# Optimization experiments

Hardware: AMD Instinct MI355X
Metric: run time of the kernel (lower is better)

## Reference

```python
import jax, jax.numpy as jnp
import numpy as np

G = 0.001
EPS = 1e-6


def setup_inputs() -> dict:
    key = jax.random.key(0)
    k1, k2 = jax.random.split(key)
    B, N, D = 8, 4096, 3
    q = jax.random.normal(k1, (B, N, D), dtype=jnp.float32)
    m = jax.random.uniform(k2, (N,), dtype=jnp.float32)
    return {"q": q, "m": m}


def reference(q, m):
    # q: (B, N, D), m: (N,)
    N = q.shape[-2]
    diff = q[:, :, None, :] - q[:, None, :, :]          # (B, N, N, D)
    dist = jnp.sqrt(jnp.sum(diff * diff, axis=-1) + EPS)  # (B, N, N)
    mass_matrix = m[:, None] * m[None, :]                # (N, N)
    V = -G * mass_matrix / dist                          # (B, N, N)
    # zero the diagonal (self-interaction), matching fill_(0.0)
    off_diag = 1.0 - jnp.eye(N, dtype=q.dtype)
    V = V * off_diag
    return jnp.sum(V, axis=(-1, -2)) / 2.0               # (B,)
```

## Files before the change

### kernel.cpp

```cpp
#include <hip/hip_runtime.h>

typedef float v4f __attribute__((ext_vector_type(4)));

#define BLK 256
#define IPT 8
#define TI (BLK * IPT)
#define TJ 64
#define JBT (TI / TJ)
#define G_CONST 0.001f
#define EPS_CONST 1e-6f

__global__ __launch_bounds__(BLK, 4)
void grav_kernel(const float* __restrict__ q, const float* __restrict__ m,
                 float* __restrict__ out, int N) {
  const int b   = blockIdx.z;
  const int tid = threadIdx.x;

  int rel = blockIdx.x;
  int a = 0;
  while (rel >= JBT * (a + 1)) { rel -= JBT * (a + 1); ++a; }
  const int jt   = rel;
  const bool diag = (jt >= JBT * a);
  const int i0 = a * TI;
  const int j0 = jt * TJ;

  __shared__ float xs[TJ], ys[TJ], zs[TJ], sjs[TJ], ms[TJ];
  __shared__ float wsum[4];

  const float* qb = q + (size_t)b * N * 3;

  if (tid < TJ) {
    const int j = j0 + tid;
    const float x = qb[3 * j + 0];
    const float y = qb[3 * j + 1];
    const float z = qb[3 * j + 2];
    xs[tid]  = x;
    ys[tid]  = y;
    zs[tid]  = z;
    sjs[tid] = fmaf(x, x, fmaf(y, y, z * z));
    ms[tid]  = m[j];
  }

  float txi[IPT], tyi[IPT], tzi[IPT], se[IPT], mi[IPT];
#pragma unroll
  for (int s = 0; s < IPT; ++s) {
    const int i = i0 + s * BLK + tid;
    const float x = qb[3 * i + 0];
    const float y = qb[3 * i + 1];
    const float z = qb[3 * i + 2];
    txi[s] = -2.f * x;
    tyi[s] = -2.f * y;
    tzi[s] = -2.f * z;
    se[s]  = fmaf(x, x, fmaf(y, y, fmaf(z, z, EPS_CONST)));
    mi[s]  = m[i];
  }

  __syncthreads();

  float acc[IPT] = {};

  if (diag) {
    for (int k = 0; k < TJ; k += 4) {
      const v4f xj = *(const v4f*)&xs[k];
      const v4f yj = *(const v4f*)&ys[k];
      const v4f zj = *(const v4f*)&zs[k];
      const v4f sj = *(const v4f*)&sjs[k];
      const v4f mj = *(const v4f*)&ms[k];
#pragma unroll
      for (int s = 0; s < IPT; ++s) {
        const int i = i0 + s * BLK + tid;
#pragma unroll
        for (int u = 0; u < 4; ++u) {
          float t = se[s] + sj[u];
          t = fmaf(txi[s], xj[u], t);
          t = fmaf(tyi[s], yj[u], t);
          t = fmaf(tzi[s], zj[u], t);
          float ri = __builtin_amdgcn_rsqf(t);
          ri = (i == j0 + k + u) ? 0.f : ri;
          acc[s] = fmaf(mj[u], ri, acc[s]);
        }
      }
    }
  } else {
    for (int k = 0; k < TJ; k += 4) {
      const v4f xj = *(const v4f*)&xs[k];
      const v4f yj = *(const v4f*)&ys[k];
      const v4f zj = *(const v4f*)&zs[k];
      const v4f sj = *(const v4f*)&sjs[k];
      const v4f mj = *(const v4f*)&ms[k];
#pragma unroll
      for (int s = 0; s < IPT; ++s) {
#pragma unroll
        for (int u = 0; u < 4; ++u) {
          float t = se[s] + sj[u];
          t = fmaf(txi[s], xj[u], t);
          t = fmaf(tyi[s], yj[u], t);
          t = fmaf(tzi[s], zj[u], t);
          acc[s] = fmaf(mj[u], __builtin_amdgcn_rsqf(t), acc[s]);
        }
      }
    }
  }

  float tsum = 0.f;
#pragma unroll
  for (int s = 0; s < IPT; ++s) tsum += mi[s] * acc[s];

#pragma unroll
  for (int off = 32; off > 0; off >>= 1) tsum += __shfl_down(tsum, off);
  const int wid  = tid >> 6;
  const int lane = tid & 63;
  if (lane == 0) wsum[wid] = tsum;
  __syncthreads();
  if (tid == 0) {
    const float s = (wsum[0] + wsum[1]) + (wsum[2] + wsum[3]);
    const float scale = diag ? (-0.5f * G_CONST) : (-G_CONST);
    atomicAdd(out + b, s * scale);
  }
}

extern "C" void kernel_launch(void* const* d_in, const int* in_sizes, int n_in,
                              void* d_out, int out_size, void* d_ws, size_t ws_size,
                              hipStream_t stream) {
  const float* q = (const float*)d_in[0];
  const float* m = (const float*)d_in[1];
  float* out = (float*)d_out;

  const int N = in_sizes[1];
  const int B = in_sizes[0] / (N * 3);

  hipMemsetAsync(out, 0, (size_t)out_size * sizeof(float), stream);

  const int nti = N / TI;
  const int bpb = JBT * nti * (nti + 1) / 2;
  dim3 grid(bpb, 1, B);
  grav_kernel<<<grid, BLK, 0, stream>>>(q, m, out, N);
}
```

Before: 33.94 us.

## Exploit pair symmetry at 256-row slot granularity inside diagonal tiles

Replaces the triangular 1D block enumeration with a full 2D (i-tile, j-tile) grid. Blocks lying entirely above the diagonal exit early. Diagonal blocks skip every 256-row slot whose rows are all below the j-tile, and a per-64-row weight of 0.5 or 1 replaces the old per-block scale to avoid double counting. This should cut roughly a third of the pairwise rsqrt work in the triangular region. In exchange, block work becomes uneven, some launched blocks do nothing, and the weighting rule is subtle to get right.

```diff
diff --git a/kernel.cpp b/kernel.cpp
--- a/kernel.cpp
+++ b/kernel.cpp
@@ -3,10 +3,9 @@
 typedef float v4f __attribute__((ext_vector_type(4)));
 
 #define BLK 256
-#define IPT 8
-#define TI (BLK * IPT)
+#define SLOTS 8
+#define TI (BLK * SLOTS)
 #define TJ 64
-#define JBT (TI / TJ)
 #define G_CONST 0.001f
 #define EPS_CONST 1e-6f
 
@@ -15,14 +14,13 @@
                  float* __restrict__ out, int N) {
   const int b   = blockIdx.z;
   const int tid = threadIdx.x;
+  const int i0  = blockIdx.x * TI;
+  const int j0  = blockIdx.y * TJ;
 
-  int rel = blockIdx.x;
-  int a = 0;
-  while (rel >= JBT * (a + 1)) { rel -= JBT * (a + 1); ++a; }
-  const int jt   = rel;
-  const bool diag = (jt >= JBT * a);
-  const int i0 = a * TI;
-  const int j0 = jt * TJ;
+  const int d     = j0 - i0;
+  const int s_min = d > 0 ? (d >> 8) : 0;
+  if (s_min >= SLOTS) return;
+  const bool has_diag = (d >= 0);
 
   __shared__ float xs[TJ], ys[TJ], zs[TJ], sjs[TJ], ms[TJ];
   __shared__ float wsum[4];
@@ -41,10 +39,13 @@
     ms[tid]  = m[j];
   }
 
-  float txi[IPT], tyi[IPT], tzi[IPT], se[IPT], mi[IPT];
+  const int jslot_end = ((j0 >> 8) + 1) << 8;
+  float txi[SLOTS], tyi[SLOTS], tzi[SLOTS], se[SLOTS], mie[SLOTS];
+  int   ii[SLOTS];
 #pragma unroll
-  for (int s = 0; s < IPT; ++s) {
+  for (int s = 0; s < SLOTS; ++s) {
     const int i = i0 + s * BLK + tid;
+    ii[s] = i;
     const float x = qb[3 * i + 0];
     const float y = qb[3 * i + 1];
     const float z = qb[3 * i + 2];
@@ -52,14 +53,15 @@
     tyi[s] = -2.f * y;
     tzi[s] = -2.f * z;
     se[s]  = fmaf(x, x, fmaf(y, y, fmaf(z, z, EPS_CONST)));
-    mi[s]  = m[i];
+    const float w = ((i & ~63) < jslot_end) ? 0.5f : 1.0f;
+    mie[s] = m[i] * w;
   }
 
   __syncthreads();
 
-  float acc[IPT] = {};
+  float acc[SLOTS] = {};
 
-  if (diag) {
+  if (has_diag) {
     for (int k = 0; k < TJ; k += 4) {
       const v4f xj = *(const v4f*)&xs[k];
       const v4f yj = *(const v4f*)&ys[k];
@@ -67,8 +69,8 @@
       const v4f sj = *(const v4f*)&sjs[k];
       const v4f mj = *(const v4f*)&ms[k];
 #pragma unroll
-      for (int s = 0; s < IPT; ++s) {
-        const int i = i0 + s * BLK + tid;
+      for (int s = 0; s < SLOTS; ++s) {
+        if (s < s_min) continue;
 #pragma unroll
         for (int u = 0; u < 4; ++u) {
           float t = se[s] + sj[u];
@@ -76,7 +78,7 @@
           t = fmaf(tyi[s], yj[u], t);
           t = fmaf(tzi[s], zj[u], t);
           float ri = __builtin_amdgcn_rsqf(t);
-          ri = (i == j0 + k + u) ? 0.f : ri;
+          ri = (ii[s] == j0 + k + u) ? 0.f : ri;
           acc[s] = fmaf(mj[u], ri, acc[s]);
         }
       }
@@ -89,7 +91,7 @@
       const v4f sj = *(const v4f*)&sjs[k];
       const v4f mj = *(const v4f*)&ms[k];
 #pragma unroll
-      for (int s = 0; s < IPT; ++s) {
+      for (int s = 0; s < SLOTS; ++s) {
 #pragma unroll
         for (int u = 0; u < 4; ++u) {
           float t = se[s] + sj[u];
@@ -104,7 +106,7 @@
 
   float tsum = 0.f;
 #pragma unroll
-  for (int s = 0; s < IPT; ++s) tsum += mi[s] * acc[s];
+  for (int s = 0; s < SLOTS; ++s) tsum += mie[s] * acc[s];
 
 #pragma unroll
   for (int off = 32; off > 0; off >>= 1) tsum += __shfl_down(tsum, off);
@@ -114,8 +116,7 @@
   __syncthreads();
   if (tid == 0) {
     const float s = (wsum[0] + wsum[1]) + (wsum[2] + wsum[3]);
-    const float scale = diag ? (-0.5f * G_CONST) : (-G_CONST);
-    atomicAdd(out + b, s * scale);
+    atomicAdd(out + b, s * (-G_CONST));
   }
 }
 
@@ -131,8 +132,6 @@
 
   hipMemsetAsync(out, 0, (size_t)out_size * sizeof(float), stream);
 
-  const int nti = N / TI;
-  const int bpb = JBT * nti * (nti + 1) / 2;
-  dim3 grid(bpb, 1, B);
+  dim3 grid(N / TI, N / TJ, B);
   grav_kernel<<<grid, BLK, 0, stream>>>(q, m, out, N);
 }
```

After: 40.37 us. +18.9%, slower.
